# Kernel optimization log

Measured on AMD Instinct MI355X. Metric: run time of the kernel, lower is better.

The kernel has to match this reference:

```python
import jax, jax.numpy as jnp
import numpy as np

L, B, C, H, K = 2048, 2, 1024, 16, 9
FF = 4 * C  # conv FFN hidden channels


def _layer_norm(x, w, b, eps=1e-5):
    mu = jnp.mean(x, axis=-1, keepdims=True)
    var = jnp.mean((x - mu) ** 2, axis=-1, keepdims=True)
    return (x - mu) * jax.lax.rsqrt(var + eps) * w + b


def setup_inputs() -> dict:
    key = jax.random.key(0)
    ks = jax.random.split(key, 8)
    s = 0.02  # init scale for weights
    return {
        "x": jax.random.normal(ks[0], (L, B, C), dtype=jnp.float32),
        "mask": jnp.zeros((B, L), dtype=bool),
        "in_proj_w": jax.random.normal(ks[1], (3 * C, C), dtype=jnp.float32) * s,
        "in_proj_b": jnp.zeros((3 * C,), dtype=jnp.float32),
        "out_proj_w": jax.random.normal(ks[2], (C, C), dtype=jnp.float32) * s,
        "out_proj_b": jnp.zeros((C,), dtype=jnp.float32),
        "conv1_w": jax.random.normal(ks[3], (FF, C, K), dtype=jnp.float32) * s,
        "conv1_b": jnp.zeros((FF,), dtype=jnp.float32),
        "conv2_w": jax.random.normal(ks[4], (C, FF, 1), dtype=jnp.float32) * s,
        "conv2_b": jnp.zeros((C,), dtype=jnp.float32),
        "norm1_w": jnp.ones((C,), dtype=jnp.float32),
        "norm1_b": jnp.zeros((C,), dtype=jnp.float32),
        "norm2_w": jnp.ones((C,), dtype=jnp.float32),
        "norm2_b": jnp.zeros((C,), dtype=jnp.float32),
    }


def reference(x, mask, in_proj_w, in_proj_b, out_proj_w, out_proj_b,
              conv1_w, conv1_b, conv2_w, conv2_b,
              norm1_w, norm1_b, norm2_w, norm2_b):
    hd = C // H
    # --- self-attention ---
    qkv = x @ in_proj_w.T + in_proj_b            # (L, B, 3C)
    q, k, v = jnp.split(qkv, 3, axis=-1)

    def heads(t):  # (L, B, C) -> (B, H, L, hd)
        return t.reshape(L, B, H, hd).transpose(1, 2, 0, 3)

    q, k, v = heads(q), heads(k), heads(v)
    scores = jnp.einsum('bhqd,bhkd->bhqk', q, k) / jnp.sqrt(jnp.float32(hd))
    scores = jnp.where(mask[:, None, None, :], -jnp.inf, scores)
    attn = jax.nn.softmax(scores, axis=-1)
    ao = jnp.einsum('bhqk,bhkd->bhqd', attn, v)  # (B, H, L, hd)
    ao = ao.transpose(2, 0, 1, 3).reshape(L, B, C)
    ao = ao @ out_proj_w.T + out_proj_b
    x1 = _layer_norm(x + ao, norm1_w, norm1_b)
    # --- conv feed-forward ---
    xc = x1.transpose(1, 2, 0)                   # (B, C, L)
    dn = ('NCH', 'OIH', 'NCH')
    h = jax.lax.conv_general_dilated(xc, conv1_w, (1,), [(K // 2, K // 2)],
                                     dimension_numbers=dn)
    h = jax.nn.relu(h + conv1_b[None, :, None])
    h = jax.lax.conv_general_dilated(h, conv2_w, (1,), [(0, 0)],
                                     dimension_numbers=dn)
    h = h + conv2_b[None, :, None]
    return _layer_norm(x1 + h.transpose(2, 0, 1), norm2_w, norm2_b)
```

## Files before the change

kernel.cpp:

```cpp
#include <hip/hip_runtime.h>
#include <cstdint>
#include <cstddef>

#define LSEQ 2048
#define NB   2
#define CCH  1024
#define NHD  16
#define HDD  64
#define FFC  4096
#define KW   9
#define MROWS 4096

typedef __bf16 bf16x8 __attribute__((ext_vector_type(8)));
typedef float  floatx4 __attribute__((ext_vector_type(4)));
typedef unsigned short ushort4v __attribute__((ext_vector_type(4)));

__device__ inline unsigned short f2bf(float f) {
  union { float f; unsigned u; } v; v.f = f;
  unsigned r = v.u + 0x7FFFu + ((v.u >> 16) & 1u);
  return (unsigned short)(r >> 16);
}

__device__ inline void gload_lds16(const unsigned short* g, unsigned short* l) {
  __builtin_amdgcn_global_load_lds(
      (__attribute__((address_space(1))) unsigned int*)(g),
      (__attribute__((address_space(3))) unsigned int*)(l), 16, 0, 0);
}

__global__ void f2bf4_kernel(const float* __restrict__ in, unsigned short* __restrict__ out, int n4) {
  int idx = blockIdx.x * 256 + threadIdx.x;
  if (idx >= n4) return;
  const floatx4 v = ((const floatx4*)in)[idx];
  unsigned long long pk = (unsigned long long)f2bf(v[0]) |
                          ((unsigned long long)f2bf(v[1]) << 16) |
                          ((unsigned long long)f2bf(v[2]) << 32) |
                          ((unsigned long long)f2bf(v[3]) << 48);
  ((unsigned long long*)out)[idx] = pk;
}

__global__ __launch_bounds__(256) void repack_w1_kernel(const float* __restrict__ in,
                                                        unsigned short* __restrict__ out) {
  __shared__ unsigned short t[9216];
  const int f = blockIdx.x, tid = threadIdx.x;
  const float* src = in + (size_t)f * 9216;
#pragma unroll
  for (int rnd = 0; rnd < 9; ++rnd) {
    const int p = (rnd * 256 + tid) * 4;
    const floatx4 v = *(const floatx4*)(src + p);
#pragma unroll
    for (int e = 0; e < 4; ++e) {
      const int idx = p + e;
      const int c = idx / 9, k = idx - c * 9;
      t[k * 1024 + c] = f2bf(v[e]);
    }
  }
  __syncthreads();
  unsigned short* dst = out + (size_t)f * 9216;
#pragma unroll
  for (int rnd = 0; rnd < 9; ++rnd) {
    const int j = (rnd * 256 + tid) * 4;
    *(ushort4v*)(dst + j) = *(const ushort4v*)&t[j];
  }
}

__global__ void zero_u16(unsigned short* p, int n) {
  int idx = blockIdx.x * 256 + threadIdx.x;
  if (idx < n) p[idx] = 0;
}

__global__ __launch_bounds__(256) void transpose_v_kernel(
    const unsigned short* __restrict__ vin, unsigned short* __restrict__ vout) {
  __shared__ unsigned short t[64][65];
  const int tid = threadIdx.x;
  const int l0 = blockIdx.x * 64, bh = blockIdx.y;
  const unsigned short* src = vin + ((size_t)bh * LSEQ + l0) * HDD;
  const int rr = tid >> 4, cc = (tid & 15) * 4;
#pragma unroll
  for (int rnd = 0; rnd < 4; ++rnd) {
    const int row = rnd * 16 + rr;
    const ushort4v v = *(const ushort4v*)(src + row * HDD + cc);
#pragma unroll
    for (int e = 0; e < 4; ++e) t[row][cc + e] = v[e];
  }
  __syncthreads();
  unsigned short* dst = vout + (size_t)bh * HDD * LSEQ + l0;
#pragma unroll
  for (int rnd = 0; rnd < 4; ++rnd) {
    const int drow = rnd * 16 + rr;
    ushort4v v;
#pragma unroll
    for (int e = 0; e < 4; ++e) v[e] = t[cc + e][drow];
    *(ushort4v*)(dst + (size_t)drow * LSEQ + cc) = v;
  }
}

template <int EPI, bool KDEC, int BN>
__global__ __launch_bounds__(256) void gemm_bt(
    const unsigned short* __restrict__ A, const unsigned short* __restrict__ Bm,
    const float* __restrict__ bias, int N, int Kstride, int Klen,
    float* __restrict__ outF, float* __restrict__ outF2,
    unsigned short* __restrict__ outB,
    unsigned short* __restrict__ qb, unsigned short* __restrict__ kb,
    unsigned short* __restrict__ vb) {
  constexpr int JN = BN / 32;
  __shared__ alignas(16) unsigned short lA[128 * 32];
  __shared__ alignas(16) unsigned short lB[BN * 32];
  const int tid = threadIdx.x;
  const int m0 = blockIdx.x * 128;
  const int n0 = blockIdx.y * BN;
  const int z = blockIdx.z;
  A += (size_t)z * Klen;
  Bm += (size_t)z * Klen;
  const int wave = tid >> 6, lane = tid & 63;
  const int wm = (wave >> 1) * 64, wn = (wave & 1) * (BN / 2);
  const int l16 = lane & 15, quad = lane >> 4;
  const int fsw = (quad ^ ((l16 >> 1) & 3)) << 3;

  size_t aoff[2], boff[BN / 64];
#pragma unroll
  for (int i = 0; i < 2; ++i) {
    const int cf = i * 256 + tid;
    const int row = cf >> 2, cs = cf & 3;
    const int col = ((cs ^ ((row >> 1) & 3)) << 3);
    aoff[i] = (KDEC ? (size_t)row * 1024 : (size_t)(m0 + row) * Kstride) + col;
  }
#pragma unroll
  for (int i = 0; i < BN / 64; ++i) {
    const int cf = i * 256 + tid;
    const int row = cf >> 2, cs = cf & 3;
    const int col = ((cs ^ ((row >> 1) & 3)) << 3);
    boff[i] = (size_t)(n0 + row) * Kstride + col;
  }

  floatx4 acc[4][JN];
#pragma unroll
  for (int i = 0; i < 4; ++i)
#pragma unroll
    for (int j = 0; j < JN; ++j) acc[i][j] = (floatx4){0.f, 0.f, 0.f, 0.f};

  auto kstep = [&](const unsigned short* Ab, const unsigned short* Bb) {
    __syncthreads();
#pragma unroll
    for (int i = 0; i < 2; ++i)
      gload_lds16(Ab + aoff[i], &lA[(i * 256 + tid) * 8]);
#pragma unroll
    for (int i = 0; i < BN / 64; ++i)
      gload_lds16(Bb + boff[i], &lB[(i * 256 + tid) * 8]);
    __syncthreads();
    bf16x8 af[4], bf[JN];
#pragma unroll
    for (int i = 0; i < 4; ++i)
      af[i] = *(const bf16x8*)&lA[(wm + i * 16 + l16) * 32 + fsw];
#pragma unroll
    for (int j = 0; j < JN; ++j)
      bf[j] = *(const bf16x8*)&lB[(wn + j * 16 + l16) * 32 + fsw];
#pragma unroll
    for (int i = 0; i < 4; ++i)
#pragma unroll
      for (int j = 0; j < JN; ++j)
        acc[i][j] = __builtin_amdgcn_mfma_f32_16x16x32_bf16(af[i], bf[j], acc[i][j], 0, 0, 0);
  };

  if (KDEC) {
    for (int seg = 0; seg < KW; ++seg) {
      const unsigned short* Ab = A + (size_t)(m0 + seg * NB) * 1024;
      const unsigned short* Bb = Bm + seg * 1024;
      for (int kk = 0; kk < 1024; kk += 32) kstep(Ab + kk, Bb + kk);
    }
  } else {
    for (int k0 = 0; k0 < Klen; k0 += 32) kstep(A + k0, Bm + k0);
  }

  float* outZ = (z == 0) ? outF : outF2;
#pragma unroll
  for (int i = 0; i < 4; ++i) {
#pragma unroll
    for (int j = 0; j < JN; ++j) {
      const int colg = n0 + wn + j * 16 + l16;
      const int rbase = m0 + wm + i * 16 + quad * 4;
      const float bv = bias ? bias[colg] : 0.f;
      float vv[4];
#pragma unroll
      for (int r = 0; r < 4; ++r) vv[r] = acc[i][j][r] + bv;
      if (EPI == 1) {
#pragma unroll
        for (int r = 0; r < 4; ++r) outZ[(size_t)(rbase + r) * N + colg] = vv[r];
      } else if (EPI == 2) {
#pragma unroll
        for (int r = 0; r < 4; ++r)
          outB[(size_t)(rbase + r) * N + colg] = f2bf(fmaxf(vv[r], 0.f));
      } else {
        const int seg = colg >> 10;
        const int c = colg & 1023, h = c >> 6, d = c & 63;
        unsigned short* dst = (seg == 0) ? qb : (seg == 1) ? kb : vb;
        const float scl = (seg == 0) ? 0.125f : 1.f;
#pragma unroll
        for (int r = 0; r < 4; ++r) {
          const int row = rbase + r, l = row >> 1, b = row & 1;
          dst[(((size_t)(b * NHD + h)) * LSEQ + l) * HDD + d] = f2bf(vv[r] * scl);
        }
      }
    }
  }
}

__global__ __launch_bounds__(256) void attn_kernel(
    const unsigned short* __restrict__ qg, const unsigned short* __restrict__ kg,
    const unsigned short* __restrict__ vtg, unsigned short* __restrict__ ao) {
  __shared__ alignas(16) unsigned short lK[64 * 64];
  __shared__ alignas(16) unsigned short lV[64 * 64];
  __shared__ alignas(16) unsigned short lP[4][16 * 64];
  const int tid = threadIdx.x;
  const int wave = tid >> 6, lane = tid & 63;
  const int l16 = lane & 15, quad = lane >> 4;
  const int sw0 = ((quad ^ (l16 & 7)) << 3);
  const int sw1 = (((quad | 4) ^ (l16 & 7)) << 3);
  const int qt = blockIdx.x, h = blockIdx.y, b = blockIdx.z;
  const unsigned short* Q = qg + ((size_t)(b * NHD + h) * LSEQ) * HDD;
  const unsigned short* Kp = kg + ((size_t)(b * NHD + h) * LSEQ) * HDD;
  const unsigned short* Vt = vtg + ((size_t)(b * NHD + h) * HDD) * LSEQ;
  const int q0 = qt * 64 + wave * 16;

  const bf16x8 qa0 = *(const bf16x8*)&Q[(size_t)(q0 + l16) * HDD + quad * 8];
  const bf16x8 qa1 = *(const bf16x8*)&Q[(size_t)(q0 + l16) * HDD + 32 + quad * 8];

  float mr[4], lr[4];
  floatx4 o[4];
#pragma unroll
  for (int r = 0; r < 4; ++r) { mr[r] = -1e30f; lr[r] = 0.f; }
#pragma unroll
  for (int nb = 0; nb < 4; ++nb) o[nb] = (floatx4){0.f, 0.f, 0.f, 0.f};

  for (int kt = 0; kt < LSEQ; kt += 64) {
    __syncthreads();
#pragma unroll
    for (int i = 0; i < 2; ++i) {
      const int flat = i * 256 + tid;
      const int row = flat >> 3, cs = flat & 7;
      const int col = ((cs ^ (row & 7)) << 3);
      gload_lds16(&Kp[(size_t)(kt + row) * HDD + col], &lK[flat * 8]);
      gload_lds16(&Vt[(size_t)row * LSEQ + kt + col], &lV[flat * 8]);
    }
    __syncthreads();
    floatx4 s[4];
#pragma unroll
    for (int nb = 0; nb < 4; ++nb) {
      const bf16x8 kf0 = *(const bf16x8*)&lK[(nb * 16 + l16) * 64 + sw0];
      const bf16x8 kf1 = *(const bf16x8*)&lK[(nb * 16 + l16) * 64 + sw1];
      floatx4 t = (floatx4){0.f, 0.f, 0.f, 0.f};
      t = __builtin_amdgcn_mfma_f32_16x16x32_bf16(qa0, kf0, t, 0, 0, 0);
      t = __builtin_amdgcn_mfma_f32_16x16x32_bf16(qa1, kf1, t, 0, 0, 0);
      s[nb] = t;
    }
    float mnew[4], alpha[4];
#pragma unroll
    for (int r = 0; r < 4; ++r) {
      float mx = fmaxf(fmaxf(s[0][r], s[1][r]), fmaxf(s[2][r], s[3][r]));
      mx = fmaxf(mx, __shfl_xor(mx, 1));
      mx = fmaxf(mx, __shfl_xor(mx, 2));
      mx = fmaxf(mx, __shfl_xor(mx, 4));
      mx = fmaxf(mx, __shfl_xor(mx, 8));
      mnew[r] = fmaxf(mr[r], mx);
      alpha[r] = __expf(mr[r] - mnew[r]);
      mr[r] = mnew[r];
    }
#pragma unroll
    for (int nb = 0; nb < 4; ++nb)
#pragma unroll
      for (int r = 0; r < 4; ++r) s[nb][r] = __expf(s[nb][r] - mnew[r]);
#pragma unroll
    for (int r = 0; r < 4; ++r) {
      float sm = s[0][r] + s[1][r] + s[2][r] + s[3][r];
      sm += __shfl_xor(sm, 1);
      sm += __shfl_xor(sm, 2);
      sm += __shfl_xor(sm, 4);
      sm += __shfl_xor(sm, 8);
      lr[r] = lr[r] * alpha[r] + sm;
    }
#pragma unroll
    for (int nb = 0; nb < 4; ++nb)
#pragma unroll
      for (int r = 0; r < 4; ++r) {
        const int row = quad * 4 + r;
        const int q = nb * 2 + (l16 >> 3);
        lP[wave][row * 64 + ((q ^ (row & 7)) << 3) + (l16 & 7)] = f2bf(s[nb][r]);
        o[nb][r] *= alpha[r];
      }
    asm volatile("s_waitcnt lgkmcnt(0)" ::: "memory");
    const bf16x8 pa0 = *(const bf16x8*)&lP[wave][l16 * 64 + sw0];
    const bf16x8 pa1 = *(const bf16x8*)&lP[wave][l16 * 64 + sw1];
#pragma unroll
    for (int nb = 0; nb < 4; ++nb) {
      const bf16x8 vf0 = *(const bf16x8*)&lV[(nb * 16 + l16) * 64 + sw0];
      const bf16x8 vf1 = *(const bf16x8*)&lV[(nb * 16 + l16) * 64 + sw1];
      o[nb] = __builtin_amdgcn_mfma_f32_16x16x32_bf16(pa0, vf0, o[nb], 0, 0, 0);
      o[nb] = __builtin_amdgcn_mfma_f32_16x16x32_bf16(pa1, vf1, o[nb], 0, 0, 0);
    }
  }
#pragma unroll
  for (int nb = 0; nb < 4; ++nb)
#pragma unroll
    for (int r = 0; r < 4; ++r) {
      const float v = o[nb][r] / lr[r];
      const int lg = q0 + quad * 4 + r;
      ao[((size_t)lg * NB + b) * CCH + h * HDD + nb * 16 + l16] = f2bf(v);
    }
}

__global__ __launch_bounds__(256) void ln_kernel(
    const float* __restrict__ a, const float* __restrict__ c,
    const float* __restrict__ c2, const float* __restrict__ cbias,
    const float* __restrict__ w, const float* __restrict__ bias,
    float* __restrict__ outF, unsigned short* __restrict__ outB) {
  const int row = blockIdx.x;
  const int tid = threadIdx.x;
  const floatx4 va = *(const floatx4*)(a + (size_t)row * 1024 + tid * 4);
  const floatx4 vc = *(const floatx4*)(c + (size_t)row * 1024 + tid * 4);
  float v0 = va[0] + vc[0], v1 = va[1] + vc[1], v2 = va[2] + vc[2], v3 = va[3] + vc[3];
  if (c2) {
    const floatx4 v2c = *(const floatx4*)(c2 + (size_t)row * 1024 + tid * 4);
    v0 += v2c[0]; v1 += v2c[1]; v2 += v2c[2]; v3 += v2c[3];
  }
  if (cbias) {
    const floatx4 vb = *(const floatx4*)(cbias + tid * 4);
    v0 += vb[0]; v1 += vb[1]; v2 += vb[2]; v3 += vb[3];
  }
  float s = v0 + v1 + v2 + v3;
  float ss = v0 * v0 + v1 * v1 + v2 * v2 + v3 * v3;
#pragma unroll
  for (int off = 1; off < 64; off <<= 1) {
    s += __shfl_xor(s, off);
    ss += __shfl_xor(ss, off);
  }
  __shared__ float red[8];
  const int wave = tid >> 6, lane = tid & 63;
  if (lane == 0) { red[wave] = s; red[4 + wave] = ss; }
  __syncthreads();
  s = red[0] + red[1] + red[2] + red[3];
  ss = red[4] + red[5] + red[6] + red[7];
  const float mu = s * (1.f / 1024.f);
  const float var = ss * (1.f / 1024.f) - mu * mu;
  const float rs = rsqrtf(var + 1e-5f);
  const floatx4 wv = *(const floatx4*)(w + tid * 4);
  const floatx4 bv = *(const floatx4*)(bias + tid * 4);
  const float o0 = (v0 - mu) * rs * wv[0] + bv[0];
  const float o1 = (v1 - mu) * rs * wv[1] + bv[1];
  const float o2 = (v2 - mu) * rs * wv[2] + bv[2];
  const float o3 = (v3 - mu) * rs * wv[3] + bv[3];
  *(floatx4*)(outF + (size_t)row * 1024 + tid * 4) = (floatx4){o0, o1, o2, o3};
  if (outB) {
    unsigned long long pk = (unsigned long long)f2bf(o0) |
                            ((unsigned long long)f2bf(o1) << 16) |
                            ((unsigned long long)f2bf(o2) << 32) |
                            ((unsigned long long)f2bf(o3) << 48);
    *(unsigned long long*)(outB + (size_t)row * 1024 + tid * 4) = pk;
  }
}

extern "C" void kernel_launch(void* const* d_in, const int* in_sizes, int n_in,
                              void* d_out, int out_size, void* d_ws, size_t ws_size,
                              hipStream_t stream) {
  const float* x = (const float*)d_in[0];
  const float* wqkv = (const float*)d_in[2];
  const float* bqkv = (const float*)d_in[3];
  const float* wout = (const float*)d_in[4];
  const float* bout = (const float*)d_in[5];
  const float* w1 = (const float*)d_in[6];
  const float* b1 = (const float*)d_in[7];
  const float* w2 = (const float*)d_in[8];
  const float* b2 = (const float*)d_in[9];
  const float* n1w = (const float*)d_in[10];
  const float* n1b = (const float*)d_in[11];
  const float* n2w = (const float*)d_in[12];
  const float* n2b = (const float*)d_in[13];
  float* out = (float*)d_out;

  char* ws = (char*)d_ws;
  size_t off = 0;
  auto alloc = [&](size_t bytes) -> char* {
    char* p = ws + off;
    off += (bytes + 255) & ~(size_t)255;
    return p;
  };
  unsigned short* xb    = (unsigned short*)alloc((size_t)MROWS * 1024 * 2);
  unsigned short* wqkvb = (unsigned short*)alloc((size_t)3072 * 1024 * 2);
  unsigned short* woutb = (unsigned short*)alloc((size_t)1024 * 1024 * 2);
  unsigned short* w1p   = (unsigned short*)alloc((size_t)FFC * 9216 * 2);
  unsigned short* w2b   = (unsigned short*)alloc((size_t)1024 * FFC * 2);
  unsigned short* qbuf  = (unsigned short*)alloc((size_t)NB * NHD * LSEQ * HDD * 2);
  unsigned short* kbuf  = (unsigned short*)alloc((size_t)NB * NHD * LSEQ * HDD * 2);
  unsigned short* vtbuf = (unsigned short*)alloc((size_t)NB * NHD * LSEQ * HDD * 2);
  unsigned short* ao    = (unsigned short*)alloc((size_t)MROWS * 1024 * 2);
  float*          yz    = (float*)alloc((size_t)MROWS * 1024 * 4);
  float*          x1f   = (float*)alloc((size_t)MROWS * 1024 * 4);
  unsigned short* x1p   = (unsigned short*)alloc((size_t)(LSEQ + 8) * NB * 1024 * 2);
  unsigned short* hbuf  = (unsigned short*)alloc((size_t)MROWS * FFC * 2);
  if (off > ws_size) return;
  float*          yzB   = (float*)xb;
  unsigned short* vbuf  = hbuf;

  int n;
  n = MROWS * 1024 / 4; f2bf4_kernel<<<(n + 255) / 256, 256, 0, stream>>>(x, xb, n);
  n = 3072 * 1024 / 4;  f2bf4_kernel<<<(n + 255) / 256, 256, 0, stream>>>(wqkv, wqkvb, n);
  n = 1024 * 1024 / 4;  f2bf4_kernel<<<(n + 255) / 256, 256, 0, stream>>>(wout, woutb, n);
  n = 1024 * FFC / 4;   f2bf4_kernel<<<(n + 255) / 256, 256, 0, stream>>>(w2, w2b, n);
  repack_w1_kernel<<<FFC, 256, 0, stream>>>(w1, w1p);
  zero_u16<<<32, 256, 0, stream>>>(x1p, 8 * 1024);
  zero_u16<<<32, 256, 0, stream>>>(x1p + (size_t)(LSEQ + 4) * NB * 1024, 8 * 1024);

  gemm_bt<0, false, 128><<<dim3(32, 24), 256, 0, stream>>>(
      xb, wqkvb, bqkv, 3072, 1024, 1024, nullptr, nullptr, nullptr, qbuf, kbuf, vbuf);
  transpose_v_kernel<<<dim3(LSEQ / 64, NB * NHD), 256, 0, stream>>>(vbuf, vtbuf);
  attn_kernel<<<dim3(LSEQ / 64, NHD, NB), 256, 0, stream>>>(qbuf, kbuf, vtbuf, ao);
  gemm_bt<1, false, 64><<<dim3(32, 16), 256, 0, stream>>>(
      ao, woutb, bout, 1024, 1024, 1024, yz, nullptr, nullptr, nullptr, nullptr, nullptr);
  ln_kernel<<<MROWS, 256, 0, stream>>>(x, yz, nullptr, nullptr, n1w, n1b, x1f, x1p + 8 * 1024);
  gemm_bt<2, true, 128><<<dim3(32, 32), 256, 0, stream>>>(
      x1p, w1p, b1, FFC, 9216, 9216, nullptr, nullptr, hbuf, nullptr, nullptr, nullptr);
  gemm_bt<1, false, 64><<<dim3(32, 16, 2), 256, 0, stream>>>(
      hbuf, w2b, nullptr, 1024, FFC, 2048, yz, yzB, nullptr, nullptr, nullptr, nullptr);
  ln_kernel<<<MROWS, 256, 0, stream>>>(x1f, yz, yzB, b2, n2w, n2b, out, nullptr);
}
```

Before: 966.0 us.

## Add dedicated 256x256-tile pipelined GEMM kernel for conv1 im2col matmul

```diff
diff --git a/kernel.cpp b/kernel.cpp
--- a/kernel.cpp
+++ b/kernel.cpp
@@ -200,6 +200,125 @@
           dst[(((size_t)(b * NHD + h)) * LSEQ + l) * HDD + d] = f2bf(vv[r] * scl);
         }
       }
+    }
+  }
+}
+
+#define WAITV8 asm volatile("s_waitcnt vmcnt(8)" ::: "memory")
+#define WAITV4 asm volatile("s_waitcnt vmcnt(4)" ::: "memory")
+#define WAITV0 asm volatile("s_waitcnt vmcnt(0)" ::: "memory")
+#define NOWAIT ((void)0)
+#define NOSTAGE ((void)0)
+
+#define PH(p, kh, rh, STAGE, WAIT) do {                                        \
+    bf16x8 af[4], bf[4];                                                       \
+    const unsigned short* Ar_ = &lA[((p) * 2 + (kh)) * 8192];                  \
+    const unsigned short* Br_ = &lB[((p) * 2 + (kh)) * 8192];                  \
+    _Pragma("unroll")                                                          \
+    for (int i_ = 0; i_ < 4; ++i_)                                             \
+      af[i_] = *(const bf16x8*)&Ar_[(wm * 128 + (rh) * 64 + i_ * 16 + l16) * 32 + fsw]; \
+    _Pragma("unroll")                                                          \
+    for (int j_ = 0; j_ < 4; ++j_)                                             \
+      bf[j_] = *(const bf16x8*)&Br_[(wn * 64 + j_ * 16 + l16) * 32 + fsw];     \
+    STAGE;                                                                     \
+    __builtin_amdgcn_s_barrier();                                              \
+    asm volatile("s_waitcnt lgkmcnt(0)" ::: "memory");                         \
+    __builtin_amdgcn_sched_barrier(0);                                         \
+    __builtin_amdgcn_s_setprio(1);                                             \
+    _Pragma("unroll")                                                          \
+    for (int i_ = 0; i_ < 4; ++i_)                                             \
+      _Pragma("unroll")                                                        \
+      for (int j_ = 0; j_ < 4; ++j_)                                           \
+        acc[(rh) * 4 + i_][j_] = __builtin_amdgcn_mfma_f32_16x16x32_bf16(      \
+            af[i_], bf[j_], acc[(rh) * 4 + i_][j_], 0, 0, 0);                  \
+    __builtin_amdgcn_s_setprio(0);                                             \
+    WAIT;                                                                      \
+    __builtin_amdgcn_s_barrier();                                              \
+  } while (0)
+
+__global__ __launch_bounds__(512, 2) void gemm256_conv1(
+    const unsigned short* __restrict__ A,
+    const unsigned short* __restrict__ Bm,
+    const float* __restrict__ bias,
+    unsigned short* __restrict__ outB) {
+  __shared__ alignas(16) unsigned short lA[4 * 8192];
+  __shared__ alignas(16) unsigned short lB[4 * 8192];
+  const int tid = threadIdx.x;
+  const int m0 = blockIdx.x * 256, n0 = blockIdx.y * 256;
+  const int wave = tid >> 6, lane = tid & 63;
+  const int wm = wave >> 2, wn = wave & 3;
+  const int l16 = lane & 15, quad = lane >> 4;
+  const int fsw = (quad ^ ((l16 >> 1) & 3)) << 3;
+
+  unsigned int aoff[2], boff[2];
+#pragma unroll
+  for (int i = 0; i < 2; ++i) {
+    const int cf = i * 512 + tid;
+    const int row = cf >> 2, cs = cf & 3;
+    const int col = (cs ^ ((row >> 1) & 3)) << 3;
+    aoff[i] = (unsigned)(m0 + row) * 1024u + (unsigned)col;
+    boff[i] = (unsigned)(n0 + row) * 9216u + (unsigned)col;
+  }
+
+  floatx4 acc[8][4];
+#pragma unroll
+  for (int i = 0; i < 8; ++i)
+#pragma unroll
+    for (int j = 0; j < 4; ++j) acc[i][j] = (floatx4){0.f, 0.f, 0.f, 0.f};
+
+  auto stA = [&](int t, int kh) {
+    const int p = t & 1;
+    const unsigned koff = (unsigned)(t >> 4) * 2048u + (unsigned)((t & 15) * 64 + kh * 32);
+#pragma unroll
+    for (int i = 0; i < 2; ++i)
+      gload_lds16(A + aoff[i] + koff, &lA[(p * 2 + kh) * 8192 + (i * 512 + tid) * 8]);
+  };
+  auto stB = [&](int t, int kh) {
+    const int p = t & 1;
+    const unsigned koff = (unsigned)t * 64u + (unsigned)(kh * 32);
+#pragma unroll
+    for (int i = 0; i < 2; ++i)
+      gload_lds16(Bm + boff[i] + koff, &lB[(p * 2 + kh) * 8192 + (i * 512 + tid) * 8]);
+  };
+
+  stA(0, 0); stB(0, 0); stA(0, 1); stB(0, 1); stA(1, 0); stB(1, 0);
+  WAITV8;
+  __builtin_amdgcn_s_barrier();
+
+  const int NIT = 72;
+  for (int it = 0; it < NIT - 1; ++it) {
+    const int T = it * 2;
+    PH(0, 0, 0, stA(T + 1, 1), NOWAIT);
+    PH(0, 0, 1, stB(T + 1, 1), WAITV8);
+    PH(0, 1, 0, stA(T + 2, 0), NOWAIT);
+    PH(0, 1, 1, stB(T + 2, 0), WAITV8);
+    PH(1, 0, 0, stA(T + 2, 1), NOWAIT);
+    PH(1, 0, 1, stB(T + 2, 1), WAITV8);
+    PH(1, 1, 0, stA(T + 3, 0), NOWAIT);
+    PH(1, 1, 1, stB(T + 3, 0), WAITV8);
+  }
+  {
+    const int T = (NIT - 1) * 2;
+    PH(0, 0, 0, stA(T + 1, 1), NOWAIT);
+    PH(0, 0, 1, stB(T + 1, 1), WAITV8);
+    PH(0, 1, 0, NOSTAGE, NOWAIT);
+    PH(0, 1, 1, NOSTAGE, WAITV4);
+    PH(1, 0, 0, NOSTAGE, NOWAIT);
+    PH(1, 0, 1, NOSTAGE, WAITV0);
+    PH(1, 1, 0, NOSTAGE, NOWAIT);
+    PH(1, 1, 1, NOSTAGE, NOWAIT);
+  }
+
+#pragma unroll
+  for (int ii = 0; ii < 8; ++ii) {
+#pragma unroll
+    for (int j = 0; j < 4; ++j) {
+      const int colg = n0 + wn * 64 + j * 16 + l16;
+      const int rbase = m0 + wm * 128 + ii * 16 + quad * 4;
+      const float bv = bias[colg];
+#pragma unroll
+      for (int r = 0; r < 4; ++r)
+        outB[(size_t)(rbase + r) * FFC + colg] = f2bf(fmaxf(acc[ii][j][r] + bv, 0.f));
     }
   }
 }
@@ -415,8 +534,7 @@
   gemm_bt<1, false, 64><<<dim3(32, 16), 256, 0, stream>>>(
       ao, woutb, bout, 1024, 1024, 1024, yz, nullptr, nullptr, nullptr, nullptr, nullptr);
   ln_kernel<<<MROWS, 256, 0, stream>>>(x, yz, nullptr, nullptr, n1w, n1b, x1f, x1p + 8 * 1024);
-  gemm_bt<2, true, 128><<<dim3(32, 32), 256, 0, stream>>>(
-      x1p, w1p, b1, FFC, 9216, 9216, nullptr, nullptr, hbuf, nullptr, nullptr, nullptr);
+  gemm256_conv1<<<dim3(16, 16), 512, 0, stream>>>(x1p, w1p, b1, hbuf);
   gemm_bt<1, false, 64><<<dim3(32, 16, 2), 256, 0, stream>>>(
       hbuf, w2b, nullptr, 1024, FFC, 2048, yz, yzB, nullptr, nullptr, nullptr, nullptr);
   ln_kernel<<<MROWS, 256, 0, stream>>>(x1f, yz, yzB, b2, n2w, n2b, out, nullptr);
```

Result: faster. 851.6 us (-11.8%).
